# Kernel tuning notes

Hardware: AMD Instinct MI355X
Metric: run time of the kernel (lower is better)

The kernel has to match this reference:

```python
import jax, jax.numpy as jnp
import numpy as np

B, S = 128, 128
AH, VH, TH = 64, 64, 128  # audio/vision/text LSTM hidden sizes
FUSED = (AH + 1) * (VH + 1) * (TH + 1)  # 545025
PF = 128  # post_fusion_dim


def setup_inputs() -> dict:
    key = jax.random.key(0)
    ks = jax.random.split(key, 6)
    return {
        "audio_h": jax.random.normal(ks[0], (B, S, AH), jnp.float32),
        "vision_h": jax.random.normal(ks[1], (B, S, VH), jnp.float32),
        "text_h": jax.random.normal(ks[2], (B, S, TH), jnp.float32),
        "W1": jax.random.normal(ks[3], (PF, FUSED), jnp.float32) * 0.001,
        "b1": jnp.zeros((PF,), jnp.float32),
        "W2": jax.random.normal(ks[4], (PF, PF), jnp.float32) * 0.05,
        "b2": jnp.zeros((PF,), jnp.float32),
        "W3": jax.random.normal(ks[5], (1, PF), jnp.float32) * 0.05,
        "b3": jnp.zeros((1,), jnp.float32),
    }


def reference(audio_h, vision_h, text_h, W1, b1, W2, b2, W3, b3):
    b, s = audio_h.shape[0], audio_h.shape[1]
    ones = jnp.ones((b, s, 1), audio_h.dtype)
    a = jnp.concatenate([ones, audio_h], axis=2)   # [B,S,AH+1]
    v = jnp.concatenate([ones, vision_h], axis=2)  # [B,S,VH+1]
    t = jnp.concatenate([ones, text_h], axis=2)    # [B,S,TH+1]
    # sum_t outer(a_t, v_t, t_t): one fused contraction over the time axis
    fusion = jnp.einsum('bsa,bsv,bsw->bavw', a, v, t)  # [B,AH+1,VH+1,TH+1]
    fusion = fusion.reshape(b, -1)                      # matches torch view order (a,v,t)
    # T2FN low-rank regularizer scale
    tmp = jnp.sqrt(jnp.asarray(AH * VH * TH / max(AH, VH, TH), jnp.float32))
    # post-fusion MLP (dropout p=0 -> identity)
    y1 = jax.nn.relu(fusion @ W1.T + b1)
    y2 = jax.nn.relu(y1 @ W2.T + b2)
    out = y2 @ W3.T + b3  # [B,1]
    out = jax.nn.sigmoid(out) * 6.0 - 3.0  # output_range=6, output_shift=-3
    norm = jnp.linalg.norm(fusion, axis=1)  # [B]
    reg_loss = jnp.mean(tmp * norm)
    return (out, reg_loss)
```

## Files before the change

kernel.cpp:

```cpp
#include <hip/hip_runtime.h>
#include <math.h>

#define BB 128
#define SS 128
#define AE 65
#define VE 65
#define TE 129
#define PFD 128
#define FUSED 545025UL
#define FUSEDI 545025
#define VSTRIDE 136
#define APLANE 8840
#define FPP 574976UL
#define FPPI 574976
#define KSP 512
#define NBLK 1123

typedef _Float16 half8 __attribute__((ext_vector_type(8)));
typedef float f32x16 __attribute__((ext_vector_type(16)));

__device__ __forceinline__ void gll16(const void* g, void* l) {
  __builtin_amdgcn_global_load_lds((const __attribute__((address_space(1))) void*)g,
                                   (__attribute__((address_space(3))) void*)l, 16, 0, 0);
}

__global__ __launch_bounds__(256) void k_zero(float* __restrict__ p, int n) {
  int i = blockIdx.x * 256 + threadIdx.x;
  if (i < n) p[i] = 0.f;
}

__global__ __launch_bounds__(256) void k_fpad(_Float16* __restrict__ Fh) {
  const int b = blockIdx.x;
  _Float16* base = Fh + (size_t)b * FPP;
  for (int i = threadIdx.x; i < 29575; i += 256) {
    const int a = i / 455, r = i - a * 455;
    const int v = r / 7, e = r - v * 7;
    base[a * APLANE + v * VSTRIDE + 129 + e] = (_Float16)0.f;
  }
  for (int i = threadIdx.x; i < 376; i += 256) base[574600 + i] = (_Float16)0.f;
}

__global__ __launch_bounds__(256) void k_core(
    const float* __restrict__ audio, const float* __restrict__ vision,
    const float* __restrict__ text, _Float16* __restrict__ Fh,
    float* __restrict__ normsq)
{
  const int b  = blockIdx.x;
  const int gy = blockIdx.y;
  const int gz = blockIdx.z;
  const int tid = threadIdx.x;
  const int wv = tid >> 6, ln = tid & 63;
  const int lr = ln & 31, hb = ln >> 5;

  __shared__ float    sVt[64][132];
  __shared__ float    sAc[8][132];
  __shared__ _Float16 sTh[64][136];
  __shared__ _Float16 sTl[64][136];

  {
    const float* vb = vision + (size_t)b * SS * 64;
#pragma unroll
    for (int r = 0; r < 32; ++r) {
      const int e = tid + 256 * r;
      sVt[e & 63][e >> 6] = vb[e];
    }
    const float* ab = audio + (size_t)b * SS * 64 + 8 * gy;
#pragma unroll
    for (int r = 0; r < 4; ++r) {
      const int e = tid + 256 * r;
      sAc[e & 7][e >> 3] = ab[(e >> 3) * 64 + (e & 7)];
    }
    const int wbase = 64 * gz;
    const float* tb = text + (size_t)b * SS * 128;
#pragma unroll
    for (int r = 0; r < 32; ++r) {
      const int e = tid + 256 * r;
      const int s = e >> 6, wl = e & 63;
      const int w = wbase + wl;
      const float val = (w == 0) ? 1.f : tb[s * 128 + w - 1];
      const _Float16 th = (_Float16)val;
      sTh[wl][s] = th;
      sTl[wl][s] = (_Float16)((val - (float)th) * 2048.f);
    }
  }
  __syncthreads();

  float ss = 0.f;
  for (int i = 0; i < 8; ++i) {
    const int u  = 8 * wv + i;
    const int rt = u >> 1, wt = u & 1;
    const int j  = rt >> 1, vh = rt & 1;
    const int v0m = 32 * vh;
    const int wl0 = 32 * wt;

    f32x16 acc = {}, accl = {};
#pragma unroll
    for (int ks = 0; ks < 8; ++ks) {
      const int s0 = 16 * ks + 8 * hb;
      const float4 x0 = *(const float4*)&sVt[v0m + lr][s0];
      const float4 x1 = *(const float4*)&sVt[v0m + lr][s0 + 4];
      const float4 a0 = *(const float4*)&sAc[j][s0];
      const float4 a1 = *(const float4*)&sAc[j][s0 + 4];
      const float pp[8] = {a0.x * x0.x, a0.y * x0.y, a0.z * x0.z, a0.w * x0.w,
                           a1.x * x1.x, a1.y * x1.y, a1.z * x1.z, a1.w * x1.w};
      half8 afh, afl;
#pragma unroll
      for (int e = 0; e < 8; ++e) {
        const _Float16 h = (_Float16)pp[e];
        afh[e] = h;
        afl[e] = (_Float16)((pp[e] - (float)h) * 2048.f);
      }
      const half8 bqh = *(const half8*)&sTh[wl0 + lr][s0];
      const half8 bql = *(const half8*)&sTl[wl0 + lr][s0];
      acc  = __builtin_amdgcn_mfma_f32_32x32x16_f16(afh, bqh, acc,  0, 0, 0);
      accl = __builtin_amdgcn_mfma_f32_32x32x16_f16(afl, bqh, accl, 0, 0, 0);
      accl = __builtin_amdgcn_mfma_f32_32x32x16_f16(afh, bql, accl, 0, 0, 0);
    }

    const int a = 1 + 8 * gy + j;
    _Float16* Fb = Fh + (size_t)b * FPP + (size_t)a * APLANE;
    const int wg = 64 * gz + wl0 + lr;
#pragma unroll
    for (int reg = 0; reg < 16; ++reg) {
      const int crow = (reg & 3) + 8 * (reg >> 2) + 4 * hb;
      const int v = 1 + 32 * vh + crow;
      const float f = acc[reg] + accl[reg] * (1.f / 2048.f);
      ss += f * f;
      Fb[(size_t)v * VSTRIDE + wg] = (_Float16)f;
    }
  }

#pragma unroll
  for (int off = 32; off > 0; off >>= 1) ss += __shfl_down(ss, off);
  if (ln == 0) atomicAdd(&normsq[b], ss);
}

__global__ __launch_bounds__(256) void k_pa(
    const float* __restrict__ vision, const float* __restrict__ text,
    _Float16* __restrict__ Fh, float* __restrict__ normsq)
{
  const int b = blockIdx.x;
  const int tid = threadIdx.x;
  const int tw = tid & 15, tv = tid >> 4;
  __shared__ float sv[32][80];
  __shared__ float st[32][144];
  float acc[5][9];
#pragma unroll
  for (int i = 0; i < 5; ++i)
#pragma unroll
    for (int j = 0; j < 9; ++j) acc[i][j] = 0.f;

  for (int c = 0; c < 4; ++c) {
    const int s0 = 32 * c;
    __syncthreads();
    const float* vbase = &vision[((size_t)(b * SS + s0)) * 64];
#pragma unroll
    for (int r = 0; r < 8; ++r) {
      const int e = tid + 256 * r;
      sv[e >> 6][(e & 63) + 1] = vbase[e];
    }
    const float* tbase = &text[((size_t)(b * SS + s0)) * 128];
#pragma unroll
    for (int r = 0; r < 16; ++r) {
      const int e = tid + 256 * r;
      st[e >> 7][(e & 127) + 1] = tbase[e];
    }
    if (tid < 32) { sv[tid][0] = 1.f; st[tid][0] = 1.f; }
    __syncthreads();
    for (int s = 0; s < 32; ++s) {
      float vr[5], tr[9];
#pragma unroll
      for (int i = 0; i < 5; ++i) {
        const int vx = tv + 16 * i;
        vr[i] = (vx < VE) ? sv[s][vx] : 0.f;
      }
#pragma unroll
      for (int j = 0; j < 9; ++j) {
        const int wx = tw + 16 * j;
        tr[j] = (wx < TE) ? st[s][wx] : 0.f;
      }
#pragma unroll
      for (int i = 0; i < 5; ++i)
#pragma unroll
        for (int j = 0; j < 9; ++j) acc[i][j] += vr[i] * tr[j];
    }
  }
  _Float16* Fb = Fh + (size_t)b * FPP;
  float ss = 0.f;
#pragma unroll
  for (int i = 0; i < 5; ++i) {
    const int v = tv + 16 * i;
    if (v < VE) {
#pragma unroll
      for (int j = 0; j < 9; ++j) {
        const int w = tw + 16 * j;
        if (w < TE) {
          const float m = acc[i][j];
          Fb[(size_t)v * VSTRIDE + w] = (_Float16)m;
          ss += m * m;
        }
      }
    }
  }
#pragma unroll
  for (int off = 32; off > 0; off >>= 1) ss += __shfl_down(ss, off);
  if ((tid & 63) == 0) atomicAdd(&normsq[b], ss);
}

__global__ __launch_bounds__(256) void k_pv(
    const float* __restrict__ audio, const float* __restrict__ text,
    _Float16* __restrict__ Fh, float* __restrict__ normsq)
{
  const int b = blockIdx.x;
  const int tid = threadIdx.x;
  const int tw = tid & 15, tv = tid >> 4;
  __shared__ float sa[32][64];
  __shared__ float st[32][144];
  float acc[4][9];
#pragma unroll
  for (int i = 0; i < 4; ++i)
#pragma unroll
    for (int j = 0; j < 9; ++j) acc[i][j] = 0.f;

  for (int c = 0; c < 4; ++c) {
    const int s0 = 32 * c;
    __syncthreads();
    const float* abase = &audio[((size_t)(b * SS + s0)) * 64];
#pragma unroll
    for (int r = 0; r < 8; ++r) {
      const int e = tid + 256 * r;
      sa[e >> 6][e & 63] = abase[e];
    }
    const float* tbase = &text[((size_t)(b * SS + s0)) * 128];
#pragma unroll
    for (int r = 0; r < 16; ++r) {
      const int e = tid + 256 * r;
      st[e >> 7][(e & 127) + 1] = tbase[e];
    }
    if (tid < 32) st[tid][0] = 1.f;
    __syncthreads();
    for (int s = 0; s < 32; ++s) {
      float ar[4], tr[9];
#pragma unroll
      for (int i = 0; i < 4; ++i) ar[i] = sa[s][tv + 16 * i];
#pragma unroll
      for (int j = 0; j < 9; ++j) {
        const int wx = tw + 16 * j;
        tr[j] = (wx < TE) ? st[s][wx] : 0.f;
      }
#pragma unroll
      for (int i = 0; i < 4; ++i)
#pragma unroll
        for (int j = 0; j < 9; ++j) acc[i][j] += ar[i] * tr[j];
    }
  }
  float ss = 0.f;
#pragma unroll
  for (int i = 0; i < 4; ++i) {
    const int a = 1 + tv + 16 * i;
    _Float16* Fb = Fh + (size_t)b * FPP + (size_t)a * APLANE;
#pragma unroll
    for (int j = 0; j < 9; ++j) {
      const int w = tw + 16 * j;
      if (w < TE) {
        const float m = acc[i][j];
        Fb[w] = (_Float16)m;
        ss += m * m;
      }
    }
  }
#pragma unroll
  for (int off = 32; off > 0; off >>= 1) ss += __shfl_down(ss, off);
  if ((tid & 63) == 0) atomicAdd(&normsq[b], ss);
}

__global__ __launch_bounds__(256) void k_wlast(
    const float* __restrict__ audio, const float* __restrict__ vision,
    const float* __restrict__ text, _Float16* __restrict__ Fh,
    float* __restrict__ Flast, float* __restrict__ normsq)
{
  const int b = blockIdx.x;
  const int tid = threadIdx.x;
  const int tw = tid & 15, tv = tid >> 4;
  __shared__ float sa[32][64];
  __shared__ float sv[32][64];
  __shared__ float swt[32];
  float acc[4][4];
#pragma unroll
  for (int i = 0; i < 4; ++i)
#pragma unroll
    for (int j = 0; j < 4; ++j) acc[i][j] = 0.f;

  for (int c = 0; c < 4; ++c) {
    const int s0 = 32 * c;
    __syncthreads();
    const float* abase = &audio[((size_t)(b * SS + s0)) * 64];
    const float* vbase = &vision[((size_t)(b * SS + s0)) * 64];
#pragma unroll
    for (int r = 0; r < 8; ++r) {
      const int e = tid + 256 * r;
      sa[e >> 6][e & 63] = abase[e];
      sv[e >> 6][e & 63] = vbase[e];
    }
    if (tid < 32) swt[tid] = text[((size_t)(b * SS + s0 + tid)) * 128 + 127];
    __syncthreads();
    for (int s = 0; s < 32; ++s) {
      const float t = swt[s];
      float ar[4], vr[4];
#pragma unroll
      for (int i = 0; i < 4; ++i) ar[i] = sa[s][tv + 16 * i] * t;
#pragma unroll
      for (int j = 0; j < 4; ++j) vr[j] = sv[s][tw + 16 * j];
#pragma unroll
      for (int i = 0; i < 4; ++i)
#pragma unroll
        for (int j = 0; j < 4; ++j) acc[i][j] += ar[i] * vr[j];
    }
  }
  float ss = 0.f;
#pragma unroll
  for (int i = 0; i < 4; ++i) {
    const int a = 1 + tv + 16 * i;
    _Float16* Fb = Fh + (size_t)b * FPP + (size_t)a * APLANE;
#pragma unroll
    for (int j = 0; j < 4; ++j) {
      const int v = 1 + tw + 16 * j;
      float m = acc[i][j];
      ss += m * m;
      if (a == 64 && v == 64) { Flast[b] = m; m = 0.f; }
      Fb[(size_t)v * VSTRIDE + 128] = (_Float16)m;
    }
  }
#pragma unroll
  for (int off = 32; off > 0; off >>= 1) ss += __shfl_down(ss, off);
  if ((tid & 63) == 0) atomicAdd(&normsq[b], ss);
}

__global__ __launch_bounds__(256) void k_gemm(
    const float* __restrict__ W1, const _Float16* __restrict__ Fh,
    float* __restrict__ parts)
{
  __shared__ _Float16 sB[2][4096];

  const int tid = threadIdx.x;
  const int wv = tid >> 6, ln = tid & 63;
  const int lb = ln & 31, hb = ln >> 5;
  const int p  = (wv << 5) + lb;
  const int kp0 = blockIdx.x * KSP;
  const int kpl0 = kp0 + (hb << 3);
  const int kpl1 = kpl0 + 16;

  int w0, ko0, w1, ko1;
  {
    const int a0 = kpl0 / APLANE; const int r0 = kpl0 - a0 * APLANE;
    const int v0 = r0 / VSTRIDE;  w0 = r0 - v0 * VSTRIDE;
    ko0 = a0 * 8385 + v0 * 129 + w0;
    const int a1 = kpl1 / APLANE; const int r1 = kpl1 - a1 * APLANE;
    const int v1 = r1 / VSTRIDE;  w1 = r1 - v1 * VSTRIDE;
    ko1 = a1 * 8385 + v1 * 129 + w1;
  }

  const float* wrow = W1 + (size_t)p * FUSED;

  const int brow0 = (wv << 5) + (ln >> 2);
  const int slogB = (ln & 3) ^ ((ln >> 2) & 3);
  const _Float16* FhP0 = Fh + (size_t)brow0 * FPP + kp0 + (slogB << 3);
  const _Float16* FhP1 = FhP0 + (size_t)16 * FPP;

  f32x16 acc0 = {}, acc1 = {}, acc2 = {}, acc3 = {};
  float4 xa[4];

#define LOADA                                                              \
  {                                                                        \
    const int kc0 = (ko0 <= 545017) ? ko0 : 545008;                        \
    const int kc1 = (ko1 <= 545017) ? ko1 : 545008;                        \
    __builtin_memcpy(&xa[0], wrow + kc0, 16);                              \
    __builtin_memcpy(&xa[1], wrow + kc0 + 4, 16);                          \
    __builtin_memcpy(&xa[2], wrow + kc1, 16);                              \
    __builtin_memcpy(&xa[3], wrow + kc1 + 4, 16);                          \
    w0 += 32; if (w0 >= VSTRIDE) { w0 -= VSTRIDE; ko0 += 25; } else ko0 += 32; \
    w1 += 32; if (w1 >= VSTRIDE) { w1 -= VSTRIDE; ko1 += 25; } else ko1 += 32; \
  }

#define STAGEB(BUF, KOFF)                                                 \
  {                                                                       \
    gll16(FhP0 + (KOFF), (char*)&sB[BUF][0] + ((wv << 5) << 6));          \
    gll16(FhP1 + (KOFF), (char*)&sB[BUF][0] + (((wv << 5) + 16) << 6));   \
  }

  LOADA
  STAGEB(0, 0)
  __syncthreads();

  int buf = 0;
  for (int t = 0; t < 16; ++t) {
    half8 af0, af1;
    af0[0] = (_Float16)xa[0].x; af0[1] = (_Float16)xa[0].y;
    af0[2] = (_Float16)xa[0].z; af0[3] = (_Float16)xa[0].w;
    af0[4] = (_Float16)xa[1].x; af0[5] = (_Float16)xa[1].y;
    af0[6] = (_Float16)xa[1].z; af0[7] = (_Float16)xa[1].w;
    af1[0] = (_Float16)xa[2].x; af1[1] = (_Float16)xa[2].y;
    af1[2] = (_Float16)xa[2].z; af1[3] = (_Float16)xa[2].w;
    af1[4] = (_Float16)xa[3].x; af1[5] = (_Float16)xa[3].y;
    af1[6] = (_Float16)xa[3].z; af1[7] = (_Float16)xa[3].w;

    if (t + 1 < 16) {
      LOADA
      STAGEB(buf ^ 1, (t + 1) * 32)
    }

    const _Float16* sBb = &sB[buf][0];
    {
      const int sl = hb;
      const char* bbase = (const char*)sBb + (lb << 6) + ((sl ^ (lb & 3)) << 4);
      const half8 b0 = *(const half8*)(bbase);
      const half8 b1 = *(const half8*)(bbase + 2048);
      const half8 b2 = *(const half8*)(bbase + 4096);
      const half8 b3 = *(const half8*)(bbase + 6144);
      acc0 = __builtin_amdgcn_mfma_f32_32x32x16_f16(af0, b0, acc0, 0, 0, 0);
      acc1 = __builtin_amdgcn_mfma_f32_32x32x16_f16(af0, b1, acc1, 0, 0, 0);
      acc2 = __builtin_amdgcn_mfma_f32_32x32x16_f16(af0, b2, acc2, 0, 0, 0);
      acc3 = __builtin_amdgcn_mfma_f32_32x32x16_f16(af0, b3, acc3, 0, 0, 0);
    }
    {
      const int sl = 2 + hb;
      const char* bbase = (const char*)sBb + (lb << 6) + ((sl ^ (lb & 3)) << 4);
      const half8 b0 = *(const half8*)(bbase);
      const half8 b1 = *(const half8*)(bbase + 2048);
      const half8 b2 = *(const half8*)(bbase + 4096);
      const half8 b3 = *(const half8*)(bbase + 6144);
      acc0 = __builtin_amdgcn_mfma_f32_32x32x16_f16(af1, b0, acc0, 0, 0, 0);
      acc1 = __builtin_amdgcn_mfma_f32_32x32x16_f16(af1, b1, acc1, 0, 0, 0);
      acc2 = __builtin_amdgcn_mfma_f32_32x32x16_f16(af1, b2, acc2, 0, 0, 0);
      acc3 = __builtin_amdgcn_mfma_f32_32x32x16_f16(af1, b3, acc3, 0, 0, 0);
    }
    __syncthreads();
    buf ^= 1;
  }
#undef LOADA
#undef STAGEB

  f32x16* o = (f32x16*)(parts + ((size_t)blockIdx.x * 256 + tid) * 64);
  o[0] = acc0; o[1] = acc1; o[2] = acc2; o[3] = acc3;
}

__global__ __launch_bounds__(256) void k_red(const float* __restrict__ parts,
                                             float* __restrict__ y1pre)
{
  const int tid = threadIdx.x;
  const int T = blockIdx.x * 4 + (tid >> 6);
  const int R = tid & 63;
  float s = 0.f;
  for (int sl = blockIdx.y; sl < NBLK; sl += 16)
    s += parts[(size_t)sl * 16384 + T * 64 + R];
  const int wv2 = T >> 6, hb2 = (T >> 5) & 1, lb2 = T & 31;
  const int q = R >> 4, rg = R & 15;
  const int b = q * 32 + lb2;
  const int pp = wv2 * 32 + (rg & 3) + 8 * (rg >> 2) + 4 * hb2;
  atomicAdd(&y1pre[b * PFD + pp], s);
}

__global__ __launch_bounds__(128) void k_final(
    const float* __restrict__ y1pre, const float* __restrict__ b1,
    const float* __restrict__ W2, const float* __restrict__ b2,
    const float* __restrict__ W3, const float* __restrict__ b3,
    const float* __restrict__ W1, const float* __restrict__ Flast,
    float* __restrict__ out)
{
  const int b = blockIdx.x, p = threadIdx.x;
  __shared__ float y1[PFD];
  __shared__ float red[PFD];
  const float extra = W1[(size_t)p * FUSED + (FUSED - 1)] * Flast[b];
  y1[p] = fmaxf(y1pre[(size_t)b * PFD + p] + extra + b1[p], 0.f);
  __syncthreads();
  float s = b2[p];
  for (int k = 0; k < PFD; ++k) s += y1[k] * W2[p * PFD + k];
  const float y2 = fmaxf(s, 0.f);
  red[p] = y2 * W3[p];
  __syncthreads();
  for (int off = 64; off > 0; off >>= 1) {
    if (p < off) red[p] += red[p + off];
    __syncthreads();
  }
  if (p == 0) {
    const float x = red[0] + b3[0];
    out[b] = 6.f / (1.f + expf(-x)) - 3.f;
  }
}

__global__ __launch_bounds__(128) void k_reg(const float* __restrict__ normsq,
                                             float* __restrict__ out)
{
  const int t = threadIdx.x;
  __shared__ float red[BB];
  red[t] = sqrtf(normsq[t]);
  __syncthreads();
  for (int off = 64; off > 0; off >>= 1) {
    if (t < off) red[t] += red[t + off];
    __syncthreads();
  }
  if (t == 0) out[BB] = 64.f * red[0] / (float)BB;
}

extern "C" void kernel_launch(void* const* d_in, const int* in_sizes, int n_in,
                              void* d_out, int out_size, void* d_ws, size_t ws_size,
                              hipStream_t stream) {
  const float* audio  = (const float*)d_in[0];
  const float* vision = (const float*)d_in[1];
  const float* text   = (const float*)d_in[2];
  const float* W1     = (const float*)d_in[3];
  const float* b1     = (const float*)d_in[4];
  const float* W2     = (const float*)d_in[5];
  const float* b2     = (const float*)d_in[6];
  const float* W3     = (const float*)d_in[7];
  const float* b3     = (const float*)d_in[8];
  float* out = (float*)d_out;

  float* y1pre  = (float*)d_ws;
  float* normsq = y1pre + BB * PFD;
  float* Flast  = normsq + BB;
  _Float16* Fh  = (_Float16*)((char*)d_ws + 131072);
  float* parts  = (float*)((char*)d_ws + 147324928);

  k_zero<<<65, 256, 0, stream>>>(y1pre, BB * PFD + 2 * BB);
  k_fpad<<<BB, 256, 0, stream>>>(Fh);

  k_core<<<dim3(BB, 8, 2), 256, 0, stream>>>(audio, vision, text, Fh, normsq);
  k_pa<<<BB, 256, 0, stream>>>(vision, text, Fh, normsq);
  k_pv<<<BB, 256, 0, stream>>>(audio, text, Fh, normsq);
  k_wlast<<<BB, 256, 0, stream>>>(audio, vision, text, Fh, Flast, normsq);

  k_gemm<<<NBLK, 256, 0, stream>>>(W1, Fh, parts);
  k_red<<<dim3(64, 16), 256, 0, stream>>>(parts, y1pre);

  k_final<<<BB, PFD, 0, stream>>>(y1pre, b1, W2, b2, W3, b3, W1, Flast, out);
  k_reg<<<1, BB, 0, stream>>>(normsq, out);
}
```

Before: 375.4 us.

## Triple-buffer LDS staging in GEMM with manual vmcnt waits and single barrier

The W1×fusion GEMM kernel goes from double to triple-buffered LDS staging of the fusion operand. It now prefetches two k-steps ahead. The main loop is fully unrolled into steps, each doing an explicit s_waitcnt vmcnt(2) and one raw s_barrier instead of a trailing __syncthreads, so the newest B tile stays in flight while the current one is consumed. This aims to hide global-load latency better and to drop one full barrier-plus-drain per iteration. In exchange it uses more LDS and relies on hand-counted outstanding-load counts, which is fragile if the compiler changes how LOADA is split into loads.

```diff
diff --git a/kernel.cpp b/kernel.cpp
--- a/kernel.cpp
+++ b/kernel.cpp
@@ -340,7 +340,7 @@
     const float* __restrict__ W1, const _Float16* __restrict__ Fh,
     float* __restrict__ parts)
 {
-  __shared__ _Float16 sB[2][4096];
+  __shared__ _Float16 sB[3][4096];
 
   const int tid = threadIdx.x;
   const int wv = tid >> 6, ln = tid & 63;
@@ -388,55 +388,74 @@
     gll16(FhP1 + (KOFF), (char*)&sB[BUF][0] + (((wv << 5) + 16) << 6));   \
   }
 
+#define GSTEP(T, WSTR)                                                         \
+  {                                                                            \
+    asm volatile("s_waitcnt " WSTR ::: "memory");                              \
+    __builtin_amdgcn_sched_barrier(0);                                         \
+    __builtin_amdgcn_s_barrier();                                              \
+    __builtin_amdgcn_sched_barrier(0);                                         \
+    half8 af0, af1;                                                            \
+    af0[0] = (_Float16)xa[0].x; af0[1] = (_Float16)xa[0].y;                    \
+    af0[2] = (_Float16)xa[0].z; af0[3] = (_Float16)xa[0].w;                    \
+    af0[4] = (_Float16)xa[1].x; af0[5] = (_Float16)xa[1].y;                    \
+    af0[6] = (_Float16)xa[1].z; af0[7] = (_Float16)xa[1].w;                    \
+    af1[0] = (_Float16)xa[2].x; af1[1] = (_Float16)xa[2].y;                    \
+    af1[2] = (_Float16)xa[2].z; af1[3] = (_Float16)xa[2].w;                    \
+    af1[4] = (_Float16)xa[3].x; af1[5] = (_Float16)xa[3].y;                    \
+    af1[6] = (_Float16)xa[3].z; af1[7] = (_Float16)xa[3].w;                    \
+    if ((T) + 1 < 16) { LOADA }                                                \
+    if ((T) + 2 < 16) { STAGEB(((T) + 2) % 3, ((T) + 2) * 32) }                \
+    __builtin_amdgcn_sched_barrier(0);                                         \
+    {                                                                          \
+      const _Float16* sBb = &sB[(T) % 3][0];                                   \
+      {                                                                        \
+        const int sl = hb;                                                     \
+        const char* bbase = (const char*)sBb + (lb << 6) + ((sl ^ (lb & 3)) << 4); \
+        const half8 b0 = *(const half8*)(bbase);                               \
+        const half8 b1 = *(const half8*)(bbase + 2048);                        \
+        const half8 b2 = *(const half8*)(bbase + 4096);                        \
+        const half8 b3 = *(const half8*)(bbase + 6144);                        \
+        acc0 = __builtin_amdgcn_mfma_f32_32x32x16_f16(af0, b0, acc0, 0, 0, 0); \
+        acc1 = __builtin_amdgcn_mfma_f32_32x32x16_f16(af0, b1, acc1, 0, 0, 0); \
+        acc2 = __builtin_amdgcn_mfma_f32_32x32x16_f16(af0, b2, acc2, 0, 0, 0); \
+        acc3 = __builtin_amdgcn_mfma_f32_32x32x16_f16(af0, b3, acc3, 0, 0, 0); \
+      }                                                                        \
+      {                                                                        \
+        const int sl = 2 + hb;                                                 \
+        const char* bbase = (const char*)sBb + (lb << 6) + ((sl ^ (lb & 3)) << 4); \
+        const half8 b0 = *(const half8*)(bbase);                               \
+        const half8 b1 = *(const half8*)(bbase + 2048);                        \
+        const half8 b2 = *(const half8*)(bbase + 4096);                        \
+        const half8 b3 = *(const half8*)(bbase + 6144);                        \
+        acc0 = __builtin_amdgcn_mfma_f32_32x32x16_f16(af1, b0, acc0, 0, 0, 0); \
+        acc1 = __builtin_amdgcn_mfma_f32_32x32x16_f16(af1, b1, acc1, 0, 0, 0); \
+        acc2 = __builtin_amdgcn_mfma_f32_32x32x16_f16(af1, b2, acc2, 0, 0, 0); \
+        acc3 = __builtin_amdgcn_mfma_f32_32x32x16_f16(af1, b3, acc3, 0, 0, 0); \
+      }                                                                        \
+    }                                                                          \
+  }
+
   LOADA
   STAGEB(0, 0)
-  __syncthreads();
-
-  int buf = 0;
-  for (int t = 0; t < 16; ++t) {
-    half8 af0, af1;
-    af0[0] = (_Float16)xa[0].x; af0[1] = (_Float16)xa[0].y;
-    af0[2] = (_Float16)xa[0].z; af0[3] = (_Float16)xa[0].w;
-    af0[4] = (_Float16)xa[1].x; af0[5] = (_Float16)xa[1].y;
-    af0[6] = (_Float16)xa[1].z; af0[7] = (_Float16)xa[1].w;
-    af1[0] = (_Float16)xa[2].x; af1[1] = (_Float16)xa[2].y;
-    af1[2] = (_Float16)xa[2].z; af1[3] = (_Float16)xa[2].w;
-    af1[4] = (_Float16)xa[3].x; af1[5] = (_Float16)xa[3].y;
-    af1[6] = (_Float16)xa[3].z; af1[7] = (_Float16)xa[3].w;
-
-    if (t + 1 < 16) {
-      LOADA
-      STAGEB(buf ^ 1, (t + 1) * 32)
-    }
-
-    const _Float16* sBb = &sB[buf][0];
-    {
-      const int sl = hb;
-      const char* bbase = (const char*)sBb + (lb << 6) + ((sl ^ (lb & 3)) << 4);
-      const half8 b0 = *(const half8*)(bbase);
-      const half8 b1 = *(const half8*)(bbase + 2048);
-      const half8 b2 = *(const half8*)(bbase + 4096);
-      const half8 b3 = *(const half8*)(bbase + 6144);
-      acc0 = __builtin_amdgcn_mfma_f32_32x32x16_f16(af0, b0, acc0, 0, 0, 0);
-      acc1 = __builtin_amdgcn_mfma_f32_32x32x16_f16(af0, b1, acc1, 0, 0, 0);
-      acc2 = __builtin_amdgcn_mfma_f32_32x32x16_f16(af0, b2, acc2, 0, 0, 0);
-      acc3 = __builtin_amdgcn_mfma_f32_32x32x16_f16(af0, b3, acc3, 0, 0, 0);
-    }
-    {
-      const int sl = 2 + hb;
-      const char* bbase = (const char*)sBb + (lb << 6) + ((sl ^ (lb & 3)) << 4);
-      const half8 b0 = *(const half8*)(bbase);
-      const half8 b1 = *(const half8*)(bbase + 2048);
-      const half8 b2 = *(const half8*)(bbase + 4096);
-      const half8 b3 = *(const half8*)(bbase + 6144);
-      acc0 = __builtin_amdgcn_mfma_f32_32x32x16_f16(af1, b0, acc0, 0, 0, 0);
-      acc1 = __builtin_amdgcn_mfma_f32_32x32x16_f16(af1, b1, acc1, 0, 0, 0);
-      acc2 = __builtin_amdgcn_mfma_f32_32x32x16_f16(af1, b2, acc2, 0, 0, 0);
-      acc3 = __builtin_amdgcn_mfma_f32_32x32x16_f16(af1, b3, acc3, 0, 0, 0);
-    }
-    __syncthreads();
-    buf ^= 1;
-  }
+  STAGEB(1, 32)
+
+  GSTEP(0,  "vmcnt(2)")
+  GSTEP(1,  "vmcnt(2)")
+  GSTEP(2,  "vmcnt(2)")
+  GSTEP(3,  "vmcnt(2)")
+  GSTEP(4,  "vmcnt(2)")
+  GSTEP(5,  "vmcnt(2)")
+  GSTEP(6,  "vmcnt(2)")
+  GSTEP(7,  "vmcnt(2)")
+  GSTEP(8,  "vmcnt(2)")
+  GSTEP(9,  "vmcnt(2)")
+  GSTEP(10, "vmcnt(2)")
+  GSTEP(11, "vmcnt(2)")
+  GSTEP(12, "vmcnt(2)")
+  GSTEP(13, "vmcnt(2)")
+  GSTEP(14, "vmcnt(2)")
+  GSTEP(15, "vmcnt(0)")
+#undef GSTEP
 #undef LOADA
 #undef STAGEB
 
```

Measured after the change: 382.3 us. About the same (+1.8%).
